# Kernel optimization log

Measured on AMD Instinct MI355X. Metric: run time of the kernel, lower is better.

The kernel has to match this reference:

```python
import jax, jax.numpy as jnp
import numpy as np

VOCAB = 50257
SOFT_CAP = 30.0
Z_LOSS_COEF = 1e-4
IGNORE_INDEX = -100


def setup_inputs() -> dict:
    key = jax.random.key(0)
    k1, k2, k3 = jax.random.split(key, 3)
    B, S, H = 2, 2048, 1024
    hidden = jax.random.normal(k1, (B, S, H), dtype=jnp.float32)
    lm_head_weight = jax.random.normal(k2, (VOCAB, H), dtype=jnp.float32) * 0.02
    labels = jax.random.randint(k3, (B, S), 0, VOCAB, dtype=jnp.int64)
    return {"hidden": hidden, "lm_head_weight": lm_head_weight, "labels": labels}


def reference(hidden, lm_head_weight, labels):
    # lm_head matmul: [B,S,H] x [V,H] -> [B,S,V]
    logits = jnp.einsum("bsh,vh->bsv", hidden, lm_head_weight)
    # Gemma-style tanh soft-cap
    logits = jnp.tanh(logits / SOFT_CAP) * SOFT_CAP
    # shift for next-token prediction
    shift_logits = logits[:, :-1].astype(jnp.float32)          # [B,S-1,V]
    shift_labels = labels[:, 1:]                               # [B,S-1]
    flat_logits = shift_logits.reshape(-1, VOCAB)              # [N,V]
    flat_labels = shift_labels.reshape(-1)                     # [N]
    valid = flat_labels != IGNORE_INDEX
    safe_labels = jnp.where(valid, flat_labels, 0)
    log_z = jax.nn.logsumexp(flat_logits, axis=-1)             # [N]
    picked = jnp.take_along_axis(flat_logits, safe_labels[:, None], axis=-1)[:, 0]
    nll = log_z - picked                                       # [N]
    n_valid = jnp.maximum(jnp.sum(valid), 1)
    ce = jnp.sum(jnp.where(valid, nll, 0.0)) / n_valid
    # z-loss: mean over valid tokens of logsumexp^2
    z_loss = ZLC = Z_LOSS_COEF * jnp.sum(jnp.where(valid, log_z ** 2, 0.0)) / n_valid
    return ce + z_loss
```

## Files before the change

### kernel.cpp

```cpp
#include <hip/hip_runtime.h>
#include <hip/hip_bf16.h>

#define VOCAB 50257
#define NPAD  50304
#define MROWS 4096
#define SEQ   2048
#define KDIM  1024

typedef __attribute__((ext_vector_type(4))) float f32x4;
typedef __attribute__((ext_vector_type(8))) short bf16x8;

#define AS1 __attribute__((address_space(1)))
#define AS3 __attribute__((address_space(3)))

__device__ __forceinline__ unsigned int f2bf_pair(float lo, float hi) {
  unsigned int a = __float_as_uint(lo);
  a = (a + 0x7FFFu + ((a >> 16) & 1u)) >> 16;
  unsigned int b = __float_as_uint(hi);
  b = (b + 0x7FFFu + ((b >> 16) & 1u)) >> 16;
  return a | (b << 16);
}

__global__ void cast_hidden_k(const float* __restrict__ src, uint4* __restrict__ dst) {
  int i = blockIdx.x * 256 + threadIdx.x;
  const float4* s = ((const float4*)src) + (size_t)i * 2;
  float4 a = s[0], b = s[1];
  uint4 o;
  o.x = f2bf_pair(a.x, a.y);
  o.y = f2bf_pair(a.z, a.w);
  o.z = f2bf_pair(b.x, b.y);
  o.w = f2bf_pair(b.z, b.w);
  dst[i] = o;
}

__global__ void cast_weight_k(const float* __restrict__ src, uint4* __restrict__ dst) {
  int i = blockIdx.x * 256 + threadIdx.x;
  int row = i >> 7;
  uint4 o = make_uint4(0u, 0u, 0u, 0u);
  if (row < VOCAB) {
    const float4* s = ((const float4*)src) + (size_t)i * 2;
    float4 a = s[0], b = s[1];
    o.x = f2bf_pair(a.x, a.y);
    o.y = f2bf_pair(a.z, a.w);
    o.z = f2bf_pair(b.x, b.y);
    o.w = f2bf_pair(b.z, b.w);
  }
  dst[i] = o;
}

__global__ __launch_bounds__(256) void gemm_ce_k(
    const unsigned short* __restrict__ A,
    const unsigned short* __restrict__ W,
    const int* __restrict__ labels,
    float* __restrict__ row_sum,
    float* __restrict__ picked)
{
  __shared__ __align__(16) unsigned short Asm_[128 * 32];
  __shared__ __align__(16) unsigned short Wsm_[128 * 32];

  const int bid  = blockIdx.x;
  const int mblk = bid & 31;
  const int nblk = bid >> 5;
  const int tid  = threadIdx.x;
  const int lane = tid & 63;
  const int w    = tid >> 6;
  const int wm   = w >> 1;
  const int wn   = w & 1;

  const int arow0 = mblk * 128;
  const int wrow0 = nblk * 128;

  f32x4 acc[4][4];
  const f32x4 zero = {0.f, 0.f, 0.f, 0.f};
#pragma unroll
  for (int m = 0; m < 4; ++m)
#pragma unroll
    for (int n = 0; n < 4; ++n) acc[m][n] = zero;

  const int sa_row = lane >> 2;
  const int sa_col = (lane & 3) * 8;
  const int rloc = lane & 15;
  const int kloc = (lane >> 4) * 8;

  for (int kb = 0; kb < KDIM; kb += 32) {
#pragma unroll
    for (int c = 0; c < 2; ++c) {
      const int rchunk = (c * 4 + w) * 16;
      const unsigned short* ga = A + (size_t)(arow0 + rchunk + sa_row) * KDIM + kb + sa_col;
      __builtin_amdgcn_global_load_lds((const AS1 void*)ga, (AS3 void*)(Asm_ + rchunk * 32), 16, 0, 0);
      const unsigned short* gw = W + (size_t)(wrow0 + rchunk + sa_row) * KDIM + kb + sa_col;
      __builtin_amdgcn_global_load_lds((const AS1 void*)gw, (AS3 void*)(Wsm_ + rchunk * 32), 16, 0, 0);
    }
    __syncthreads();

    bf16x8 af[4], bf[4];
#pragma unroll
    for (int m = 0; m < 4; ++m)
      af[m] = *(const bf16x8*)(Asm_ + (wm * 64 + m * 16 + rloc) * 32 + kloc);
#pragma unroll
    for (int n = 0; n < 4; ++n)
      bf[n] = *(const bf16x8*)(Wsm_ + (wn * 64 + n * 16 + rloc) * 32 + kloc);
#pragma unroll
    for (int m = 0; m < 4; ++m)
#pragma unroll
      for (int n = 0; n < 4; ++n)
        acc[m][n] = __builtin_amdgcn_mfma_f32_16x16x32_bf16(af[m], bf[n], acc[m][n], 0, 0, 0);
    __syncthreads();
  }

#pragma unroll
  for (int m = 0; m < 4; ++m) {
#pragma unroll
    for (int r = 0; r < 4; ++r) {
      const int grow = arow0 + wm * 64 + m * 16 + (lane >> 4) * 4 + r;
      int lab = -1;
      if ((grow & (SEQ - 1)) != (SEQ - 1)) lab = labels[grow + 1];
      float s = 0.f;
#pragma unroll
      for (int n = 0; n < 4; ++n) {
        const int v = wrow0 + wn * 64 + n * 16 + (lane & 15);
        const float z = acc[m][n][r];
        const float e2 = __expf(z * (2.f / 30.f));
        const float capped = 30.f * (1.f - 2.f * __builtin_amdgcn_rcpf(e2 + 1.f));
        if (v == lab) picked[grow] = capped;
        s += (v < VOCAB) ? __expf(capped) : 0.f;
      }
      s += __shfl_xor(s, 1);
      s += __shfl_xor(s, 2);
      s += __shfl_xor(s, 4);
      s += __shfl_xor(s, 8);
      if ((lane & 15) == 0) atomicAdd(&row_sum[grow], s);
    }
  }
}

__global__ void reduce_k(const int* __restrict__ labels, const float* __restrict__ row_sum,
                         const float* __restrict__ picked, float* __restrict__ out)
{
  const int tid = threadIdx.x;
  float ce = 0.f, zl = 0.f;
  int cnt = 0;
  for (int r = tid; r < MROWS; r += 256) {
    if ((r & (SEQ - 1)) == (SEQ - 1)) continue;
    const int lab = labels[r + 1];
    if (lab == -100) continue;
    const float lz = __logf(row_sum[r]);
    ce += lz - picked[r];
    zl += lz * lz;
    ++cnt;
  }
  __shared__ float sce[4], szl[4];
  __shared__ int scnt[4];
#pragma unroll
  for (int off = 32; off > 0; off >>= 1) {
    ce  += __shfl_down(ce, off);
    zl  += __shfl_down(zl, off);
    cnt += __shfl_down(cnt, off);
  }
  const int wv = tid >> 6;
  if ((tid & 63) == 0) { sce[wv] = ce; szl[wv] = zl; scnt[wv] = cnt; }
  __syncthreads();
  if (tid == 0) {
    float C = 0.f, Z = 0.f;
    int N = 0;
    for (int i = 0; i < 4; ++i) { C += sce[i]; Z += szl[i]; N += scnt[i]; }
    if (N < 1) N = 1;
    out[0] = C / N + 1e-4f * (Z / N);
  }
}

extern "C" void kernel_launch(void* const* d_in, const int* in_sizes, int n_in,
                              void* d_out, int out_size, void* d_ws, size_t ws_size,
                              hipStream_t stream) {
  const float* hidden = (const float*)d_in[0];
  const float* weight = (const float*)d_in[1];
  const int*   labels = (const int*)d_in[2];
  float* out = (float*)d_out;

  const size_t A_BYTES = (size_t)MROWS * KDIM * 2;
  const size_t W_BYTES = (size_t)NPAD * KDIM * 2;
  const size_t NEEDED  = A_BYTES + W_BYTES + 2 * MROWS * sizeof(float);
  if (ws_size < NEEDED) return;

  char* ws = (char*)d_ws;
  unsigned short* Abf = (unsigned short*)ws;
  unsigned short* Wbf = (unsigned short*)(ws + A_BYTES);
  float* row_sum = (float*)(ws + A_BYTES + W_BYTES);
  float* picked  = row_sum + MROWS;

  hipMemsetAsync(row_sum, 0, MROWS * sizeof(float), stream);
  cast_hidden_k<<<MROWS * KDIM / 8 / 256, 256, 0, stream>>>(hidden, (uint4*)Abf);
  cast_weight_k<<<NPAD * KDIM / 8 / 256, 256, 0, stream>>>(weight, (uint4*)Wbf);
  gemm_ce_k<<<32 * 393, 256, 0, stream>>>(Abf, Wbf, labels, row_sum, picked);
  reduce_k<<<1, 256, 0, stream>>>(labels, row_sum, picked, out);
}
```

Baseline: 889.9 us.

## Rewrite GEMM as 256x256 tiles with double-buffered swizzled LDS pipeline

Replaces the 128x128, K=32, single-buffered GEMM with a 256x256 tile using 512 threads and K=64 steps. LDS is double-buffered with an XOR swizzle, and global-to-LDS loads for the next stages are interleaved with MFMA phases under fine-grained barriers and s_setprio. Workgroup IDs are remapped across 8 groups, likely for XCD/L2 locality. The goal is more data reuse per byte loaded and hiding load latency behind compute, at the cost of more registers and LDS (128KB), which limits occupancy. NPAD grows so the vocab dimension divides by 256.

```diff
diff --git a/kernel.cpp b/kernel.cpp
--- a/kernel.cpp
+++ b/kernel.cpp
@@ -2,16 +2,23 @@
 #include <hip/hip_bf16.h>
 
 #define VOCAB 50257
-#define NPAD  50304
+#define NPAD  50432
 #define MROWS 4096
 #define SEQ   2048
 #define KDIM  1024
+#define NT    16
 
 typedef __attribute__((ext_vector_type(4))) float f32x4;
 typedef __attribute__((ext_vector_type(8))) short bf16x8;
 
 #define AS1 __attribute__((address_space(1)))
 #define AS3 __attribute__((address_space(3)))
+
+__device__ __forceinline__ void bar() {
+  asm volatile("" ::: "memory");
+  __builtin_amdgcn_s_barrier();
+  asm volatile("" ::: "memory");
+}
 
 __device__ __forceinline__ unsigned int f2bf_pair(float lo, float hi) {
   unsigned int a = __float_as_uint(lo);
@@ -48,78 +55,153 @@
   dst[i] = o;
 }
 
-__global__ __launch_bounds__(256) void gemm_ce_k(
+#define STAGE_X(base, h, bufb, isB, kt) do { \
+  const unsigned short* _g = (base) + (size_t)((h)*128 + w*8) * KDIM + (kt)*64; \
+  unsigned short* _l = LDS_ + (bufb) + (isB)*16384 + (h)*8192 + w*512; \
+  __builtin_amdgcn_global_load_lds((const AS1 void*)_g, (AS3 void*)_l, 16, 0, 0); \
+  __builtin_amdgcn_global_load_lds((const AS1 void*)(_g + (size_t)64*KDIM), (AS3 void*)(_l + 4096), 16, 0, 0); \
+} while (0)
+
+__global__ __launch_bounds__(512, 2) void gemm_ce_k(
     const unsigned short* __restrict__ A,
     const unsigned short* __restrict__ W,
     const int* __restrict__ labels,
     float* __restrict__ row_sum,
     float* __restrict__ picked)
 {
-  __shared__ __align__(16) unsigned short Asm_[128 * 32];
-  __shared__ __align__(16) unsigned short Wsm_[128 * 32];
+  __shared__ __align__(16) unsigned short LDS_[65536];
 
   const int bid  = blockIdx.x;
-  const int mblk = bid & 31;
-  const int nblk = bid >> 5;
+  const int wg   = (bid & 7) * 394 + (bid >> 3);
+  const int mblk = wg & 15;
+  const int nblk = wg >> 4;
   const int tid  = threadIdx.x;
   const int lane = tid & 63;
   const int w    = tid >> 6;
-  const int wm   = w >> 1;
-  const int wn   = w & 1;
-
-  const int arow0 = mblk * 128;
-  const int wrow0 = nblk * 128;
-
-  f32x4 acc[4][4];
-  const f32x4 zero = {0.f, 0.f, 0.f, 0.f};
-#pragma unroll
-  for (int m = 0; m < 4; ++m)
-#pragma unroll
-    for (int n = 0; n < 4; ++n) acc[m][n] = zero;
-
-  const int sa_row = lane >> 2;
-  const int sa_col = (lane & 3) * 8;
-  const int rloc = lane & 15;
-  const int kloc = (lane >> 4) * 8;
-
-  for (int kb = 0; kb < KDIM; kb += 32) {
-#pragma unroll
-    for (int c = 0; c < 2; ++c) {
-      const int rchunk = (c * 4 + w) * 16;
-      const unsigned short* ga = A + (size_t)(arow0 + rchunk + sa_row) * KDIM + kb + sa_col;
-      __builtin_amdgcn_global_load_lds((const AS1 void*)ga, (AS3 void*)(Asm_ + rchunk * 32), 16, 0, 0);
-      const unsigned short* gw = W + (size_t)(wrow0 + rchunk + sa_row) * KDIM + kb + sa_col;
-      __builtin_amdgcn_global_load_lds((const AS1 void*)gw, (AS3 void*)(Wsm_ + rchunk * 32), 16, 0, 0);
-    }
-    __syncthreads();
-
-    bf16x8 af[4], bf[4];
-#pragma unroll
-    for (int m = 0; m < 4; ++m)
-      af[m] = *(const bf16x8*)(Asm_ + (wm * 64 + m * 16 + rloc) * 32 + kloc);
-#pragma unroll
-    for (int n = 0; n < 4; ++n)
-      bf[n] = *(const bf16x8*)(Wsm_ + (wn * 64 + n * 16 + rloc) * 32 + kloc);
-#pragma unroll
-    for (int m = 0; m < 4; ++m)
-#pragma unroll
-      for (int n = 0; n < 4; ++n)
-        acc[m][n] = __builtin_amdgcn_mfma_f32_16x16x32_bf16(af[m], bf[n], acc[m][n], 0, 0, 0);
-    __syncthreads();
-  }
-
-#pragma unroll
-  for (int m = 0; m < 4; ++m) {
+  const int wm   = w >> 2;
+  const int wn   = w & 3;
+
+  const int arow0 = mblk * 256;
+  const int wrow0 = nblk * 256;
+
+  const int lrow = lane >> 3;
+  const int lcol = ((lane & 7) * 8) ^ ((lane >> 3) << 3);
+  const unsigned short* Abase = A + (size_t)(arow0 + lrow) * KDIM + lcol;
+  const unsigned short* Wbase = W + (size_t)(wrow0 + lrow) * KDIM + lcol;
+
+  const int rbase = (lane & 15) * 64 + (lane >> 4) * 8;
+  const int xorm  = (lane & 7) << 3;
+
+  f32x4 acc[8][4];
+#pragma unroll
+  for (int m = 0; m < 8; ++m)
+#pragma unroll
+    for (int n = 0; n < 4; ++n) acc[m][n] = (f32x4){0.f, 0.f, 0.f, 0.f};
+
+  STAGE_X(Abase, 0, 0, 0, 0);
+  STAGE_X(Abase, 1, 0, 0, 0);
+  STAGE_X(Wbase, 0, 0, 1, 0);
+  STAGE_X(Wbase, 1, 0, 1, 0);
+  STAGE_X(Abase, 0, 32768, 0, 1);
+  STAGE_X(Abase, 1, 32768, 0, 1);
+  asm volatile("s_waitcnt vmcnt(4)" ::: "memory");
+  bar();
+
+  bf16x8 Af[2][4][2], Bf[2][2][2];
+
+  for (int t = 0; t < NT; ++t) {
+    const int cb = (t & 1) << 15;
+    const int nb = cb ^ 32768;
+
+#pragma unroll
+    for (int a = 0; a < 4; ++a)
+#pragma unroll
+      for (int ks = 0; ks < 2; ++ks)
+        Af[0][a][ks] = *(const bf16x8*)&LDS_[cb + (((wm*128 + a*16)*64 + rbase + ks*32) ^ xorm)];
+#pragma unroll
+    for (int b2 = 0; b2 < 2; ++b2)
+#pragma unroll
+      for (int ks = 0; ks < 2; ++ks)
+        Bf[0][b2][ks] = *(const bf16x8*)&LDS_[cb + 16384 + (((wn*64 + b2*16)*64 + rbase + ks*32) ^ xorm)];
+    if (t + 1 < NT) STAGE_X(Wbase, 0, nb, 1, t + 1);
+    bar();
+    __builtin_amdgcn_s_setprio(1);
+#pragma unroll
+    for (int a = 0; a < 4; ++a)
+#pragma unroll
+      for (int b2 = 0; b2 < 2; ++b2) {
+        acc[a][b2] = __builtin_amdgcn_mfma_f32_16x16x32_bf16(Af[0][a][0], Bf[0][b2][0], acc[a][b2], 0, 0, 0);
+        acc[a][b2] = __builtin_amdgcn_mfma_f32_16x16x32_bf16(Af[0][a][1], Bf[0][b2][1], acc[a][b2], 0, 0, 0);
+      }
+    __builtin_amdgcn_s_setprio(0);
+    bar();
+
+#pragma unroll
+    for (int a = 0; a < 4; ++a)
+#pragma unroll
+      for (int ks = 0; ks < 2; ++ks)
+        Af[1][a][ks] = *(const bf16x8*)&LDS_[cb + (((wm*128 + 64 + a*16)*64 + rbase + ks*32) ^ xorm)];
+#pragma unroll
+    for (int b2 = 0; b2 < 2; ++b2)
+#pragma unroll
+      for (int ks = 0; ks < 2; ++ks)
+        Bf[1][b2][ks] = *(const bf16x8*)&LDS_[cb + 16384 + (((wn*64 + 32 + b2*16)*64 + rbase + ks*32) ^ xorm)];
+    if (t + 1 < NT) STAGE_X(Wbase, 1, nb, 1, t + 1);
+    bar();
+    __builtin_amdgcn_s_setprio(1);
+#pragma unroll
+    for (int a = 0; a < 4; ++a)
+#pragma unroll
+      for (int b2 = 0; b2 < 2; ++b2) {
+        acc[a][2+b2] = __builtin_amdgcn_mfma_f32_16x16x32_bf16(Af[0][a][0], Bf[1][b2][0], acc[a][2+b2], 0, 0, 0);
+        acc[a][2+b2] = __builtin_amdgcn_mfma_f32_16x16x32_bf16(Af[0][a][1], Bf[1][b2][1], acc[a][2+b2], 0, 0, 0);
+      }
+    __builtin_amdgcn_s_setprio(0);
+    bar();
+
+    if (t + 2 < NT) STAGE_X(Abase, 0, cb, 0, t + 2);
+    bar();
+    __builtin_amdgcn_s_setprio(1);
+#pragma unroll
+    for (int a = 0; a < 4; ++a)
+#pragma unroll
+      for (int b2 = 0; b2 < 2; ++b2) {
+        acc[4+a][b2] = __builtin_amdgcn_mfma_f32_16x16x32_bf16(Af[1][a][0], Bf[0][b2][0], acc[4+a][b2], 0, 0, 0);
+        acc[4+a][b2] = __builtin_amdgcn_mfma_f32_16x16x32_bf16(Af[1][a][1], Bf[0][b2][1], acc[4+a][b2], 0, 0, 0);
+      }
+    __builtin_amdgcn_s_setprio(0);
+    bar();
+
+    if (t + 2 < NT) STAGE_X(Abase, 1, cb, 0, t + 2);
+    bar();
+    __builtin_amdgcn_s_setprio(1);
+#pragma unroll
+    for (int a = 0; a < 4; ++a)
+#pragma unroll
+      for (int b2 = 0; b2 < 2; ++b2) {
+        acc[4+a][2+b2] = __builtin_amdgcn_mfma_f32_16x16x32_bf16(Af[1][a][0], Bf[1][b2][0], acc[4+a][2+b2], 0, 0, 0);
+        acc[4+a][2+b2] = __builtin_amdgcn_mfma_f32_16x16x32_bf16(Af[1][a][1], Bf[1][b2][1], acc[4+a][2+b2], 0, 0, 0);
+      }
+    __builtin_amdgcn_s_setprio(0);
+    if (t < NT - 2) { asm volatile("s_waitcnt vmcnt(4)" ::: "memory"); }
+    else           { asm volatile("s_waitcnt vmcnt(0)" ::: "memory"); }
+    bar();
+  }
+
+  const int arow_w = arow0 + wm * 128;
+  const int vcol_w = wrow0 + wn * 64;
+#pragma unroll
+  for (int m8 = 0; m8 < 8; ++m8) {
 #pragma unroll
     for (int r = 0; r < 4; ++r) {
-      const int grow = arow0 + wm * 64 + m * 16 + (lane >> 4) * 4 + r;
+      const int grow = arow_w + m8 * 16 + (lane >> 4) * 4 + r;
       int lab = -1;
       if ((grow & (SEQ - 1)) != (SEQ - 1)) lab = labels[grow + 1];
       float s = 0.f;
 #pragma unroll
-      for (int n = 0; n < 4; ++n) {
-        const int v = wrow0 + wn * 64 + n * 16 + (lane & 15);
-        const float z = acc[m][n][r];
+      for (int n4 = 0; n4 < 4; ++n4) {
+        const int v = vcol_w + n4 * 16 + (lane & 15);
+        const float z = acc[m8][n4][r];
         const float e2 = __expf(z * (2.f / 30.f));
         const float capped = 30.f * (1.f - 2.f * __builtin_amdgcn_rcpf(e2 + 1.f));
         if (v == lab) picked[grow] = capped;
@@ -191,6 +273,6 @@
   hipMemsetAsync(row_sum, 0, MROWS * sizeof(float), stream);
   cast_hidden_k<<<MROWS * KDIM / 8 / 256, 256, 0, stream>>>(hidden, (uint4*)Abf);
   cast_weight_k<<<NPAD * KDIM / 8 / 256, 256, 0, stream>>>(weight, (uint4*)Wbf);
-  gemm_ce_k<<<32 * 393, 256, 0, stream>>>(Abf, Wbf, labels, row_sum, picked);
+  gemm_ce_k<<<16 * 197 , 512, 0, stream>>>(Abf, Wbf, labels, row_sum, picked);
   reduce_k<<<1, 256, 0, stream>>>(labels, row_sum, picked, out);
 }
```

Result: slower. 947.2 us (+6.4%).
